# Performance work log

Measured on AMD Instinct MI355X. Metric: run time of the kernel, lower is better.

Reference implementation:

```python
import math
import jax, jax.numpy as jnp
import numpy as np

H = 12
D_MODEL = 768
D_K = D_MODEL // H
B, S = 2, 2048


def setup_inputs() -> dict:
    key = jax.random.key(0)
    ks = jax.random.split(key, 12)
    sc = 0.02
    inp = {
        "query": jax.random.normal(ks[0], (B, S, D_MODEL), jnp.float32),
        "key": jax.random.normal(ks[1], (B, S, D_MODEL), jnp.float32),
        "value": jax.random.normal(ks[2], (B, S, D_MODEL), jnp.float32),
        # causal mask [B, S, S]: 1 where attendable
        "mask": jnp.broadcast_to(jnp.tril(jnp.ones((S, S), jnp.int32)), (B, S, S)),
        "Wq": sc * jax.random.normal(ks[3], (D_MODEL, D_MODEL), jnp.float32),
        "bq": jnp.zeros((D_MODEL,), jnp.float32),
        "Wk": sc * jax.random.normal(ks[4], (D_MODEL, D_MODEL), jnp.float32),
        "bk": jnp.zeros((D_MODEL,), jnp.float32),
        "Wv": sc * jax.random.normal(ks[5], (D_MODEL, D_MODEL), jnp.float32),
        "bv": jnp.zeros((D_MODEL,), jnp.float32),
        "Wo": sc * jax.random.normal(ks[6], (D_MODEL, D_MODEL), jnp.float32),
        "bo": jnp.zeros((D_MODEL,), jnp.float32),
    }
    return inp


def reference(query, key, value, mask, Wq, bq, Wk, bk, Wv, bv, Wo, bo):
    b, s, _ = query.shape
    # linear projections (torch Linear: x @ W.T + b), split into heads
    def proj(x, W, bias):
        return (x @ W.T + bias).reshape(b, s, H, D_K).transpose(0, 2, 1, 3)  # [B,H,S,Dk]

    q = proj(query, Wq, bq)
    k = proj(key, Wk, bk)
    v = proj(value, Wv, bv)

    scores = jnp.einsum("bhqd,bhkd->bhqk", q, k) / math.sqrt(D_K)  # [B,H,S,S]
    # exponential time-decay bias over key positions 1..S, shape [1,1,1,S]
    time = jnp.exp(-jnp.arange(1, s + 1, dtype=scores.dtype))[None, None, None, :]
    scores = jnp.where(mask[:, None, :, :] == 0, jnp.asarray(-1e9, scores.dtype), scores)
    p_attn = jax.nn.softmax(scores - time, axis=-1)
    x = jnp.einsum("bhqk,bhkd->bhqd", p_attn, v)  # [B,H,S,Dk]
    x = x.transpose(0, 2, 1, 3).reshape(b, s, H * D_K)
    return x @ Wo.T + bo
```

## Files before the change

kernel.cpp:

```cpp
#include <hip/hip_runtime.h>
#include <hip/hip_bf16.h>
#include <math.h>

typedef __bf16 bf16;
typedef __attribute__((ext_vector_type(8))) __bf16 bf16x8;
typedef __attribute__((ext_vector_type(4))) float floatx4;

#define NH 12
#define DK 64
#define DM 768
#define NB 2
#define SEQ 2048
#define MTOT (NB * SEQ)
#define WELEM (DM * DM)

static __device__ __forceinline__ bf16x8 load8(const bf16* p) {
    return *(const bf16x8*)p;
}
static __device__ __forceinline__ float4 ld4(const float* p) {
    return *(const float4*)p;
}
static __device__ __forceinline__ bf16x8 cvt8(const float4 a, const float4 b) {
    bf16x8 r;
    r[0] = (bf16)a.x; r[1] = (bf16)a.y; r[2] = (bf16)a.z; r[3] = (bf16)a.w;
    r[4] = (bf16)b.x; r[5] = (bf16)b.y; r[6] = (bf16)b.z; r[7] = (bf16)b.w;
    return r;
}
static __device__ __forceinline__ void async16(const bf16* g, bf16* l) {
    __builtin_amdgcn_global_load_lds((const __attribute__((address_space(1))) void*)g,
                                     (__attribute__((address_space(3))) void*)l,
                                     16, 0, 0);
}

__global__ __launch_bounds__(256) void cvtw_kernel(const float* __restrict__ wq,
                                                   const float* __restrict__ wk,
                                                   const float* __restrict__ wv,
                                                   const float* __restrict__ wo,
                                                   bf16* __restrict__ dst,
                                                   bf16* __restrict__ wob) {
    const int g = blockIdx.x * 256 + threadIdx.x;
    const int PW = WELEM / 8;
    const int wi = g / PW;
    const int rem = g - wi * PW;
    const int n = rem / 96;
    const int t = rem - n * 96;
    const int s = t >> 3;
    const int j = t & 7;
    const float* src = (wi == 0) ? wq : (wi == 1) ? wk : (wi == 2) ? wv : wo;
    bf16* dbase = (wi < 3) ? (dst + (size_t)wi * WELEM) : wob;
    const float* p = src + (size_t)n * DM + s * 64 + j * 8;
    bf16* d = dbase + (size_t)n * DM + s * 64 + ((j ^ (n & 7)) * 8);
    *(bf16x8*)d = cvt8(ld4(p), ld4(p + 4));
}

__global__ __launch_bounds__(256, 3) void qkv_kernel(
    const float* __restrict__ Xq, const float* __restrict__ Xk, const float* __restrict__ Xv,
    const bf16* __restrict__ Wb,
    const float* __restrict__ bq, const float* __restrict__ bk, const float* __restrict__ bv,
    bf16* __restrict__ Oq, bf16* __restrict__ Ok, bf16* __restrict__ Ov) {
    __shared__ bf16 As[128][72];
    __shared__ bf16 Bs[2][128 * 64];

    const int tid = threadIdx.x;
    const int id = blockIdx.x;
    const int xcd = id & 7;
    const int sl = id >> 3;
    const int z = sl / 24;
    const int rr = sl % 24;
    const int m0 = (xcd * 4 + rr / 6) * 128;
    const int n0 = (rr % 6) * 128;

    const float* X = (z == 0) ? Xq : (z == 1) ? Xk : Xv;
    const bf16* W = Wb + (size_t)z * WELEM;
    const float* bias = (z == 0) ? bq : (z == 1) ? bk : bv;
    bf16* out = (z == 0) ? Oq : (z == 1) ? Ok : Ov;
    const int omode = (z == 2) ? 1 : 0;

    const int wv = tid >> 6;
    const int wm = wv >> 1, wn = wv & 1;
    const int lane = tid & 63;
    const int ln = lane & 15;
    const int kq = lane >> 4;
    const int arow = tid >> 1;
    const int acol = (tid & 1) * 32;

    const float* xbase = &X[(size_t)(m0 + arow) * DM + acol];
    const int brow_l = lane >> 3;
    const int bcol_l = (lane & 7) * 8;

    floatx4 acc[4][4];
#pragma unroll
    for (int i = 0; i < 4; i++)
#pragma unroll
        for (int j = 0; j < 4; j++) acc[i][j] = (floatx4){0.f, 0.f, 0.f, 0.f};

    float4 ax[8];
#pragma unroll
    for (int q = 0; q < 8; q++) ax[q] = ld4(xbase + q * 4);
#pragma unroll
    for (int it = 0; it < 4; it++) {
        const bf16* g = W + (size_t)(n0 + it * 32 + wv * 8 + brow_l) * DM + bcol_l;
        async16(g, &Bs[0][(it * 32 + wv * 8) * 64]);
    }

    for (int k = 0; k < 12; k++) {
        const int k0 = k * 64;
        __syncthreads();
        *(bf16x8*)&As[arow][acol]      = cvt8(ax[0], ax[1]);
        *(bf16x8*)&As[arow][acol + 8]  = cvt8(ax[2], ax[3]);
        *(bf16x8*)&As[arow][acol + 16] = cvt8(ax[4], ax[5]);
        *(bf16x8*)&As[arow][acol + 24] = cvt8(ax[6], ax[7]);
        __syncthreads();
        if (k < 11) {
            const float* xp = xbase + k0 + 64;
#pragma unroll
            for (int q = 0; q < 8; q++) ax[q] = ld4(xp + q * 4);
            const int p = (k + 1) & 1;
#pragma unroll
            for (int it = 0; it < 4; it++) {
                const bf16* g = W + (size_t)(n0 + it * 32 + wv * 8 + brow_l) * DM + (k0 + 64) + bcol_l;
                async16(g, &Bs[p][(it * 32 + wv * 8) * 64]);
            }
        }
        const bf16* Bp = &Bs[k & 1][0];
#pragma unroll
        for (int ks = 0; ks < 2; ks++) {
            bf16x8 af[4], bfm[4];
#pragma unroll
            for (int mt = 0; mt < 4; mt++) af[mt] = *(bf16x8*)&As[wm * 64 + mt * 16 + ln][ks * 32 + kq * 8];
#pragma unroll
            for (int nt = 0; nt < 4; nt++) {
                const int brow = wn * 64 + nt * 16 + ln;
                const int jb = (ks * 4 + kq) ^ (ln & 7);
                bfm[nt] = *(const bf16x8*)&Bp[brow * 64 + jb * 8];
            }
#pragma unroll
            for (int mt = 0; mt < 4; mt++)
#pragma unroll
                for (int nt = 0; nt < 4; nt++)
                    acc[mt][nt] = __builtin_amdgcn_mfma_f32_16x16x32_bf16(af[mt], bfm[nt], acc[mt][nt], 0, 0, 0);
        }
    }

    bf16 (*E)[136] = (bf16(*)[136])As;
    float bv4[4];
#pragma unroll
    for (int nt = 0; nt < 4; nt++) bv4[nt] = bias[n0 + wn * 64 + nt * 16 + ln];
    const int erow = tid >> 2;
    const int ecol = (tid & 3) * 32;

    if (omode == 0) {
        const int b = m0 >> 11;
#pragma unroll
        for (int half = 0; half < 2; half++) {
            __syncthreads();
            if (wm == half) {
#pragma unroll
                for (int mt = 0; mt < 4; mt++)
#pragma unroll
                    for (int nt = 0; nt < 4; nt++)
#pragma unroll
                        for (int r2 = 0; r2 < 4; r2++)
                            E[mt * 16 + kq * 4 + r2][wn * 64 + nt * 16 + ln] = (bf16)(acc[mt][nt][r2] + bv4[nt]);
            }
            __syncthreads();
            const int m = m0 + half * 64 + erow;
            const int ss = m & (SEQ - 1);
#pragma unroll
            for (int g = 0; g < 2; g++) {
                const int c = ecol + g * 16;
                const int n = n0 + c;
                const int h = n >> 6, d = n & 63;
                bf16* op = &out[((size_t)(b * NH + h) * SEQ + ss) * DK + d];
                *(bf16x8*)op = *(bf16x8*)&E[erow][c];
                *(bf16x8*)(op + 8) = *(bf16x8*)&E[erow][c + 8];
            }
        }
    } else {
        const int b = m0 >> 11;
        const int s0 = m0 & (SEQ - 1);
#pragma unroll
        for (int half = 0; half < 2; half++) {
            __syncthreads();
            if (wn == half) {
#pragma unroll
                for (int nt = 0; nt < 4; nt++)
#pragma unroll
                    for (int mt = 0; mt < 4; mt++) {
#pragma unroll
                        for (int r2 = 0; r2 < 4; r2++)
                            E[nt * 16 + ln][wm * 64 + mt * 16 + kq * 4 + r2] = (bf16)(acc[mt][nt][r2] + bv4[nt]);
                    }
            }
            __syncthreads();
            const int n = n0 + half * 64 + erow;
            const int h = n >> 6, d = n & 63;
            bf16* op = &out[(size_t)(b * NH + h) * DK * SEQ + (size_t)d * SEQ + s0 + ecol];
            *(bf16x8*)op = *(bf16x8*)&E[erow][ecol];
            *(bf16x8*)(op + 8) = *(bf16x8*)&E[erow][ecol + 8];
            *(bf16x8*)(op + 16) = *(bf16x8*)&E[erow][ecol + 16];
            *(bf16x8*)(op + 24) = *(bf16x8*)&E[erow][ecol + 24];
        }
    }
}

__global__ __launch_bounds__(256) void attn_kernel(const bf16* __restrict__ Q,
                                                   const bf16* __restrict__ K,
                                                   const bf16* __restrict__ Vt,
                                                   bf16* __restrict__ Xout) {
    __shared__ bf16 Ks[128][72];
    __shared__ bf16 Vs[64][136];
    __shared__ bf16 Ps[4][16][136];

    const int tid = threadIdx.x;
    const int wv = tid >> 6;
    const int lane = tid & 63;
    const int ln = lane & 15;
    const int kq = lane >> 4;
    const int krow = tid >> 1;
    const int kcol = (tid & 1) * 32;
    const int vrow = tid >> 2;
    const int vcol = (tid & 3) * 32;

    const int bidx = blockIdx.x;
    const int rk = (bidx < 256 || bidx >= 512) ? bidx : 767 - bidx;
    const int x = 31 - (rk / 24);
    const int bh = rk % 24;

    const int q0 = x * 64;
    const int qbase = q0 + wv * 16;
    const int nch = (x >> 1) + 1;

    const bf16* Qb = Q + (size_t)bh * SEQ * DK;
    const bf16* Kb = K + (size_t)bh * SEQ * DK;
    const bf16* Vb = Vt + (size_t)bh * SEQ * DK;

    const bf16x8 qa0 = load8(&Qb[(size_t)(qbase + ln) * DK + kq * 8]);
    const bf16x8 qa1 = load8(&Qb[(size_t)(qbase + ln) * DK + 32 + kq * 8]);

    bf16x8 kx[4], vx[4];
#pragma unroll
    for (int q = 0; q < 4; q++) {
        kx[q] = load8(&Kb[(size_t)krow * DK + kcol + q * 8]);
        vx[q] = load8(&Vb[(size_t)vrow * SEQ + vcol + q * 8]);
    }

    float lsum[4] = {0.f, 0.f, 0.f, 0.f};
    floatx4 Oacc[4];
#pragma unroll
    for (int nt = 0; nt < 4; nt++) Oacc[nt] = (floatx4){0.f, 0.f, 0.f, 0.f};

    int qg[4];
#pragma unroll
    for (int r = 0; r < 4; r++) qg[r] = qbase + kq * 4 + r;

    for (int c = 0; c < nch; c++) {
        const int k0 = c * 128;
        __syncthreads();
#pragma unroll
        for (int q = 0; q < 4; q++) {
            *(bf16x8*)&Ks[krow][kcol + q * 8] = kx[q];
            *(bf16x8*)&Vs[vrow][vcol + q * 8] = vx[q];
        }
        __syncthreads();
        if (c + 1 < nch) {
            const int kn = k0 + 128;
#pragma unroll
            for (int q = 0; q < 4; q++) {
                kx[q] = load8(&Kb[(size_t)(kn + krow) * DK + kcol + q * 8]);
                vx[q] = load8(&Vb[(size_t)vrow * SEQ + kn + vcol + q * 8]);
            }
        }

        floatx4 sc[8];
#pragma unroll
        for (int ks = 0; ks < 8; ks++) {
            const bf16x8 b0 = *(bf16x8*)&Ks[ks * 16 + ln][kq * 8];
            const bf16x8 b1 = *(bf16x8*)&Ks[ks * 16 + ln][32 + kq * 8];
            floatx4 t = (floatx4){0.f, 0.f, 0.f, 0.f};
            t = __builtin_amdgcn_mfma_f32_16x16x32_bf16(qa0, b0, t, 0, 0, 0);
            t = __builtin_amdgcn_mfma_f32_16x16x32_bf16(qa1, b1, t, 0, 0, 0);
            sc[ks] = t;
        }

        const bool last = (c == nch - 1);
#pragma unroll
        for (int ks = 0; ks < 8; ks++) {
            const int kg = k0 + ks * 16 + ln;
            const float tb = __expf(-(float)(kg + 1));
#pragma unroll
            for (int r = 0; r < 4; r++) {
                const float sv = sc[ks][r] * 0.125f - tb;
                float pf = __expf(sv);
                if (last && kg > qg[r]) pf = 0.f;
                const bf16 pb = (bf16)pf;
                Ps[wv][kq * 4 + r][ks * 16 + ln] = pb;
                lsum[r] += (float)pb;
            }
        }

        bf16x8 pa[4];
#pragma unroll
        for (int seg = 0; seg < 4; seg++) pa[seg] = *(bf16x8*)&Ps[wv][ln][seg * 32 + kq * 8];
#pragma unroll
        for (int nt = 0; nt < 4; nt++) {
#pragma unroll
            for (int seg = 0; seg < 4; seg++) {
                const bf16x8 vb = *(bf16x8*)&Vs[nt * 16 + ln][seg * 32 + kq * 8];
                Oacc[nt] = __builtin_amdgcn_mfma_f32_16x16x32_bf16(pa[seg], vb, Oacc[nt], 0, 0, 0);
            }
        }
    }

#pragma unroll
    for (int off = 1; off < 16; off <<= 1) {
#pragma unroll
        for (int r = 0; r < 4; r++) lsum[r] += __shfl_xor(lsum[r], off, 64);
    }
    float rl[4];
#pragma unroll
    for (int r = 0; r < 4; r++) rl[r] = 1.f / lsum[r];

    __syncthreads();
    bf16 (*E)[72] = (bf16(*)[72])Ks;
    const int erow = tid >> 2;
    const int ecb = (tid & 3) * 16;
#pragma unroll
    for (int nt = 0; nt < 4; nt++) {
#pragma unroll
        for (int r = 0; r < 4; r++)
            E[wv * 16 + kq * 4 + r][nt * 16 + ln] = (bf16)(Oacc[nt][r] * rl[r]);
    }
    __syncthreads();
    const int b = bh / NH;
    const int h = bh - b * NH;
    const int q = q0 + erow;
    bf16* op = &Xout[((size_t)(b * SEQ + q)) * DM + h * DK + ecb];
    *(bf16x8*)op = *(bf16x8*)&E[erow][ecb];
    *(bf16x8*)(op + 8) = *(bf16x8*)&E[erow][ecb + 8];
}

__global__ __launch_bounds__(256, 3) void outproj_kernel(const bf16* __restrict__ X,
                                                         const bf16* __restrict__ W,
                                                         const float* __restrict__ bias,
                                                         float* __restrict__ out) {
    __shared__ bf16 As[128][72];
    __shared__ bf16 Bs[2][128 * 64];

    const int tid = threadIdx.x;
    const int id = blockIdx.x;
    const int xcd = id & 7;
    const int sl = id >> 3;
    const int m0 = (xcd * 4 + sl / 6) * 128;
    const int n0 = (sl % 6) * 128;

    const int wv = tid >> 6;
    const int wm = wv >> 1, wn = wv & 1;
    const int lane = tid & 63;
    const int ln = lane & 15;
    const int kq = lane >> 4;
    const int arow = tid >> 1;
    const int acol = (tid & 1) * 32;

    const bf16* xbase = &X[(size_t)(m0 + arow) * DM + acol];
    const int brow_l = lane >> 3;
    const int bcol_l = (lane & 7) * 8;

    floatx4 acc[4][4];
#pragma unroll
    for (int i = 0; i < 4; i++)
#pragma unroll
        for (int j = 0; j < 4; j++) acc[i][j] = (floatx4){0.f, 0.f, 0.f, 0.f};

    bf16x8 ax[4];
#pragma unroll
    for (int q = 0; q < 4; q++) ax[q] = load8(xbase + q * 8);
#pragma unroll
    for (int it = 0; it < 4; it++) {
        const bf16* g = W + (size_t)(n0 + it * 32 + wv * 8 + brow_l) * DM + bcol_l;
        async16(g, &Bs[0][(it * 32 + wv * 8) * 64]);
    }

    for (int k = 0; k < 12; k++) {
        const int k0 = k * 64;
        __syncthreads();
        *(bf16x8*)&As[arow][acol]      = ax[0];
        *(bf16x8*)&As[arow][acol + 8]  = ax[1];
        *(bf16x8*)&As[arow][acol + 16] = ax[2];
        *(bf16x8*)&As[arow][acol + 24] = ax[3];
        __syncthreads();
        if (k < 11) {
            const bf16* xp = xbase + k0 + 64;
#pragma unroll
            for (int q = 0; q < 4; q++) ax[q] = load8(xp + q * 8);
            const int p = (k + 1) & 1;
#pragma unroll
            for (int it = 0; it < 4; it++) {
                const bf16* g = W + (size_t)(n0 + it * 32 + wv * 8 + brow_l) * DM + (k0 + 64) + bcol_l;
                async16(g, &Bs[p][(it * 32 + wv * 8) * 64]);
            }
        }
        const bf16* Bp = &Bs[k & 1][0];
#pragma unroll
        for (int ks = 0; ks < 2; ks++) {
            bf16x8 af[4], bfm[4];
#pragma unroll
            for (int mt = 0; mt < 4; mt++) af[mt] = *(bf16x8*)&As[wm * 64 + mt * 16 + ln][ks * 32 + kq * 8];
#pragma unroll
            for (int nt = 0; nt < 4; nt++) {
                const int brow = wn * 64 + nt * 16 + ln;
                const int jb = (ks * 4 + kq) ^ (ln & 7);
                bfm[nt] = *(const bf16x8*)&Bp[brow * 64 + jb * 8];
            }
#pragma unroll
            for (int mt = 0; mt < 4; mt++)
#pragma unroll
                for (int nt = 0; nt < 4; nt++)
                    acc[mt][nt] = __builtin_amdgcn_mfma_f32_16x16x32_bf16(af[mt], bfm[nt], acc[mt][nt], 0, 0, 0);
        }
    }

#pragma unroll
    for (int nt = 0; nt < 4; nt++) {
        const int n = n0 + wn * 64 + nt * 16 + ln;
        const float bval = bias[n];
#pragma unroll
        for (int mt = 0; mt < 4; mt++)
#pragma unroll
            for (int r2 = 0; r2 < 4; r2++) {
                const int m = m0 + wm * 64 + mt * 16 + kq * 4 + r2;
                out[(size_t)m * DM + n] = acc[mt][nt][r2] + bval;
            }
    }
}

extern "C" void kernel_launch(void* const* d_in, const int* in_sizes, int n_in,
                              void* d_out, int out_size, void* d_ws, size_t ws_size,
                              hipStream_t stream) {
    const float* query = (const float*)d_in[0];
    const float* key   = (const float*)d_in[1];
    const float* value = (const float*)d_in[2];
    const float* Wq = (const float*)d_in[4];
    const float* bq = (const float*)d_in[5];
    const float* Wk = (const float*)d_in[6];
    const float* bk = (const float*)d_in[7];
    const float* Wv = (const float*)d_in[8];
    const float* bv = (const float*)d_in[9];
    const float* Wo = (const float*)d_in[10];
    const float* bo = (const float*)d_in[11];
    float* out = (float*)d_out;

    const size_t nElem = (size_t)NB * NH * SEQ * DK;
    bf16* Qws  = (bf16*)d_ws;
    bf16* Kws  = Qws + nElem;
    bf16* Vtws = Kws + nElem;
    bf16* Xws  = Vtws + nElem;
    bf16* Wob  = Xws + (size_t)MTOT * DM;

    bf16* Wb = (bf16*)out;

    cvtw_kernel<<<(4 * WELEM / 8) / 256, 256, 0, stream>>>(Wq, Wk, Wv, Wo, Wb, Wob);

    qkv_kernel<<<576, 256, 0, stream>>>(query, key, value, Wb, bq, bk, bv,
                                        Qws, Kws, Vtws);

    attn_kernel<<<768, 256, 0, stream>>>(Qws, Kws, Vtws, Xws);

    outproj_kernel<<<192, 256, 0, stream>>>(Xws, Wob, bo, out);
}
```

Before: 225.3 us.

## Pre-convert activations to bf16 and use async LDS loads with smaller GEMM tiles

Adds the fp32→bf16 conversion of the query/key/value activations to the weight-conversion kernel, writing them with an XOR-swizzled layout. The QKV and output-projection GEMMs can then load both operands straight into LDS with double-buffered global_load_lds, instead of going through registers with a convert step. M tiles shrink from 128 to 64, doubling the grid for better occupancy and balance. The attention epilogue now writes its output swizzled to match the outproj loader. The cost is an extra pass over the activations through workspace, plus smaller tiles that reuse each weight tile less.

```diff
diff --git a/kernel.cpp b/kernel.cpp
--- a/kernel.cpp
+++ b/kernel.cpp
@@ -4,6 +4,7 @@
 
 typedef __bf16 bf16;
 typedef __attribute__((ext_vector_type(8))) __bf16 bf16x8;
+typedef __attribute__((ext_vector_type(4))) __bf16 bf16x4;
 typedef __attribute__((ext_vector_type(4))) float floatx4;
 
 #define NH 12
@@ -13,6 +14,7 @@
 #define SEQ 2048
 #define MTOT (NB * SEQ)
 #define WELEM (DM * DM)
+#define XELEM (MTOT * DM)
 
 static __device__ __forceinline__ bf16x8 load8(const bf16* p) {
     return *(const bf16x8*)p;
@@ -32,175 +34,172 @@
                                      16, 0, 0);
 }
 
-__global__ __launch_bounds__(256) void cvtw_kernel(const float* __restrict__ wq,
-                                                   const float* __restrict__ wk,
-                                                   const float* __restrict__ wv,
-                                                   const float* __restrict__ wo,
-                                                   bf16* __restrict__ dst,
-                                                   bf16* __restrict__ wob) {
+__global__ __launch_bounds__(256) void cvt_kernel(
+    const float* __restrict__ wq, const float* __restrict__ wk,
+    const float* __restrict__ wv, const float* __restrict__ wo,
+    const float* __restrict__ xq, const float* __restrict__ xk, const float* __restrict__ xv,
+    bf16* __restrict__ Wb, bf16* __restrict__ Wob,
+    bf16* __restrict__ Xqb, bf16* __restrict__ Xkb, bf16* __restrict__ Xvb) {
     const int g = blockIdx.x * 256 + threadIdx.x;
     const int PW = WELEM / 8;
-    const int wi = g / PW;
-    const int rem = g - wi * PW;
-    const int n = rem / 96;
-    const int t = rem - n * 96;
-    const int s = t >> 3;
-    const int j = t & 7;
-    const float* src = (wi == 0) ? wq : (wi == 1) ? wk : (wi == 2) ? wv : wo;
-    bf16* dbase = (wi < 3) ? (dst + (size_t)wi * WELEM) : wob;
-    const float* p = src + (size_t)n * DM + s * 64 + j * 8;
-    bf16* d = dbase + (size_t)n * DM + s * 64 + ((j ^ (n & 7)) * 8);
-    *(bf16x8*)d = cvt8(ld4(p), ld4(p + 4));
+    const int PX = XELEM / 8;
+    if (g < 4 * PW) {
+        const int wi = g / PW;
+        const int rem = g - wi * PW;
+        const int n = rem / 96;
+        const int t = rem - n * 96;
+        const int s = t >> 3;
+        const int j = t & 7;
+        const float* src = (wi == 0) ? wq : (wi == 1) ? wk : (wi == 2) ? wv : wo;
+        bf16* dst = (wi < 3) ? (Wb + (size_t)wi * WELEM) : Wob;
+        const float* p = src + (size_t)n * DM + s * 64 + j * 8;
+        *(bf16x8*)(dst + (size_t)n * DM + s * 64 + ((j ^ (n & 7)) * 8)) = cvt8(ld4(p), ld4(p + 4));
+    } else {
+        const int gx = g - 4 * PW;
+        const int xi = gx / PX;
+        const int rem = gx - xi * PX;
+        const int m = rem / 96;
+        const int t = rem - m * 96;
+        const int s = t >> 3;
+        const int j = t & 7;
+        const float* src = (xi == 0) ? xq : (xi == 1) ? xk : xv;
+        bf16* dst = (xi == 0) ? Xqb : (xi == 1) ? Xkb : Xvb;
+        const float* p = src + (size_t)m * DM + s * 64 + j * 8;
+        *(bf16x8*)(dst + (size_t)m * DM + s * 64 + ((j ^ (m & 7)) * 8)) = cvt8(ld4(p), ld4(p + 4));
+    }
 }
 
 __global__ __launch_bounds__(256, 3) void qkv_kernel(
-    const float* __restrict__ Xq, const float* __restrict__ Xk, const float* __restrict__ Xv,
+    const bf16* __restrict__ Xqb, const bf16* __restrict__ Xkb, const bf16* __restrict__ Xvb,
     const bf16* __restrict__ Wb,
     const float* __restrict__ bq, const float* __restrict__ bk, const float* __restrict__ bv,
     bf16* __restrict__ Oq, bf16* __restrict__ Ok, bf16* __restrict__ Ov) {
-    __shared__ bf16 As[128][72];
-    __shared__ bf16 Bs[2][128 * 64];
+    __shared__ __align__(16) bf16 SM[2 * 64 * 64 + 2 * 128 * 64];
+    bf16* As0 = SM;
+    bf16* Bs0 = SM + 8192;
 
     const int tid = threadIdx.x;
     const int id = blockIdx.x;
     const int xcd = id & 7;
     const int sl = id >> 3;
-    const int z = sl / 24;
-    const int rr = sl % 24;
-    const int m0 = (xcd * 4 + rr / 6) * 128;
-    const int n0 = (rr % 6) * 128;
-
-    const float* X = (z == 0) ? Xq : (z == 1) ? Xk : Xv;
+    const int z = sl / 48;
+    const int r = sl % 48;
+    const int m0 = (xcd * 8 + r / 6) * 64;
+    const int n0 = (r % 6) * 128;
+
+    const bf16* X = (z == 0) ? Xqb : (z == 1) ? Xkb : Xvb;
     const bf16* W = Wb + (size_t)z * WELEM;
     const float* bias = (z == 0) ? bq : (z == 1) ? bk : bv;
     bf16* out = (z == 0) ? Oq : (z == 1) ? Ok : Ov;
-    const int omode = (z == 2) ? 1 : 0;
 
     const int wv = tid >> 6;
     const int wm = wv >> 1, wn = wv & 1;
     const int lane = tid & 63;
     const int ln = lane & 15;
     const int kq = lane >> 4;
-    const int arow = tid >> 1;
-    const int acol = (tid & 1) * 32;
-
-    const float* xbase = &X[(size_t)(m0 + arow) * DM + acol];
-    const int brow_l = lane >> 3;
-    const int bcol_l = (lane & 7) * 8;
-
-    floatx4 acc[4][4];
-#pragma unroll
-    for (int i = 0; i < 4; i++)
+    const int drow = lane >> 3;
+    const int dcol = (lane & 7) * 8;
+
+    floatx4 acc[2][4];
+#pragma unroll
+    for (int i = 0; i < 2; i++)
 #pragma unroll
         for (int j = 0; j < 4; j++) acc[i][j] = (floatx4){0.f, 0.f, 0.f, 0.f};
 
-    float4 ax[8];
-#pragma unroll
-    for (int q = 0; q < 8; q++) ax[q] = ld4(xbase + q * 4);
-#pragma unroll
-    for (int it = 0; it < 4; it++) {
-        const bf16* g = W + (size_t)(n0 + it * 32 + wv * 8 + brow_l) * DM + bcol_l;
-        async16(g, &Bs[0][(it * 32 + wv * 8) * 64]);
-    }
+#pragma unroll
+    for (int it = 0; it < 2; it++)
+        async16(X + (size_t)(m0 + wv * 16 + it * 8 + drow) * DM + dcol,
+                As0 + (wv * 16 + it * 8) * 64);
+#pragma unroll
+    for (int it = 0; it < 4; it++)
+        async16(W + (size_t)(n0 + wv * 32 + it * 8 + drow) * DM + dcol,
+                Bs0 + (wv * 32 + it * 8) * 64);
 
     for (int k = 0; k < 12; k++) {
-        const int k0 = k * 64;
-        __syncthreads();
-        *(bf16x8*)&As[arow][acol]      = cvt8(ax[0], ax[1]);
-        *(bf16x8*)&As[arow][acol + 8]  = cvt8(ax[2], ax[3]);
-        *(bf16x8*)&As[arow][acol + 16] = cvt8(ax[4], ax[5]);
-        *(bf16x8*)&As[arow][acol + 24] = cvt8(ax[6], ax[7]);
-        __syncthreads();
+        __syncthreads();
+        const bf16* Ap = As0 + (k & 1) * 4096;
+        const bf16* Bp = Bs0 + (k & 1) * 8192;
         if (k < 11) {
-            const float* xp = xbase + k0 + 64;
-#pragma unroll
-            for (int q = 0; q < 8; q++) ax[q] = ld4(xp + q * 4);
-            const int p = (k + 1) & 1;
-#pragma unroll
-            for (int it = 0; it < 4; it++) {
-                const bf16* g = W + (size_t)(n0 + it * 32 + wv * 8 + brow_l) * DM + (k0 + 64) + bcol_l;
-                async16(g, &Bs[p][(it * 32 + wv * 8) * 64]);
-            }
-        }
-        const bf16* Bp = &Bs[k & 1][0];
+            const int kc = (k + 1) * 64;
+            bf16* An = As0 + ((k + 1) & 1) * 4096;
+            bf16* Bn = Bs0 + ((k + 1) & 1) * 8192;
+#pragma unroll
+            for (int it = 0; it < 2; it++)
+                async16(X + (size_t)(m0 + wv * 16 + it * 8 + drow) * DM + kc + dcol,
+                        An + (wv * 16 + it * 8) * 64);
+#pragma unroll
+            for (int it = 0; it < 4; it++)
+                async16(W + (size_t)(n0 + wv * 32 + it * 8 + drow) * DM + kc + dcol,
+                        Bn + (wv * 32 + it * 8) * 64);
+        }
 #pragma unroll
         for (int ks = 0; ks < 2; ks++) {
-            bf16x8 af[4], bfm[4];
-#pragma unroll
-            for (int mt = 0; mt < 4; mt++) af[mt] = *(bf16x8*)&As[wm * 64 + mt * 16 + ln][ks * 32 + kq * 8];
-#pragma unroll
-            for (int nt = 0; nt < 4; nt++) {
-                const int brow = wn * 64 + nt * 16 + ln;
-                const int jb = (ks * 4 + kq) ^ (ln & 7);
-                bfm[nt] = *(const bf16x8*)&Bp[brow * 64 + jb * 8];
-            }
-#pragma unroll
-            for (int mt = 0; mt < 4; mt++)
+            const int jb = (ks * 4 + kq) ^ (ln & 7);
+            bf16x8 af[2], bfm[4];
+#pragma unroll
+            for (int mt = 0; mt < 2; mt++)
+                af[mt] = *(const bf16x8*)&Ap[(wm * 32 + mt * 16 + ln) * 64 + jb * 8];
+#pragma unroll
+            for (int nt = 0; nt < 4; nt++)
+                bfm[nt] = *(const bf16x8*)&Bp[(wn * 64 + nt * 16 + ln) * 64 + jb * 8];
+#pragma unroll
+            for (int mt = 0; mt < 2; mt++)
 #pragma unroll
                 for (int nt = 0; nt < 4; nt++)
                     acc[mt][nt] = __builtin_amdgcn_mfma_f32_16x16x32_bf16(af[mt], bfm[nt], acc[mt][nt], 0, 0, 0);
         }
     }
 
-    bf16 (*E)[136] = (bf16(*)[136])As;
     float bv4[4];
 #pragma unroll
     for (int nt = 0; nt < 4; nt++) bv4[nt] = bias[n0 + wn * 64 + nt * 16 + ln];
-    const int erow = tid >> 2;
-    const int ecol = (tid & 3) * 32;
-
-    if (omode == 0) {
-        const int b = m0 >> 11;
-#pragma unroll
-        for (int half = 0; half < 2; half++) {
-            __syncthreads();
-            if (wm == half) {
-#pragma unroll
-                for (int mt = 0; mt < 4; mt++)
-#pragma unroll
-                    for (int nt = 0; nt < 4; nt++)
-#pragma unroll
-                        for (int r2 = 0; r2 < 4; r2++)
-                            E[mt * 16 + kq * 4 + r2][wn * 64 + nt * 16 + ln] = (bf16)(acc[mt][nt][r2] + bv4[nt]);
+
+    if (z < 2) {
+        __syncthreads();
+        bf16 (*E)[136] = (bf16(*)[136])SM;
+#pragma unroll
+        for (int mt = 0; mt < 2; mt++)
+#pragma unroll
+            for (int nt = 0; nt < 4; nt++)
+#pragma unroll
+                for (int r2 = 0; r2 < 4; r2++)
+                    E[wm * 32 + mt * 16 + kq * 4 + r2][wn * 64 + nt * 16 + ln] =
+                        (bf16)(acc[mt][nt][r2] + bv4[nt]);
+        __syncthreads();
+        const int row = tid >> 2;
+        const int cb = (tid & 3) * 32;
+        const int m = m0 + row;
+        const int b = m >> 11;
+        const int s = m & (SEQ - 1);
+        const int h = (n0 + cb) >> 6;
+        const int d = (n0 + cb) & 63;
+        bf16* op = &out[((size_t)(b * NH + h) * SEQ + s) * DK + d];
+#pragma unroll
+        for (int q2 = 0; q2 < 4; q2++)
+            *(bf16x8*)(op + q2 * 8) = *(bf16x8*)&E[row][cb + q2 * 8];
+    } else {
+        __syncthreads();
+        bf16 (*E)[72] = (bf16(*)[72])SM;
+#pragma unroll
+        for (int nt = 0; nt < 4; nt++)
+#pragma unroll
+            for (int mt = 0; mt < 2; mt++) {
+                bf16x4 v;
+#pragma unroll
+                for (int r2 = 0; r2 < 4; r2++) v[r2] = (bf16)(acc[mt][nt][r2] + bv4[nt]);
+                *(bf16x4*)&E[wn * 64 + nt * 16 + ln][wm * 32 + mt * 16 + kq * 4] = v;
             }
-            __syncthreads();
-            const int m = m0 + half * 64 + erow;
-            const int ss = m & (SEQ - 1);
-#pragma unroll
-            for (int g = 0; g < 2; g++) {
-                const int c = ecol + g * 16;
-                const int n = n0 + c;
-                const int h = n >> 6, d = n & 63;
-                bf16* op = &out[((size_t)(b * NH + h) * SEQ + ss) * DK + d];
-                *(bf16x8*)op = *(bf16x8*)&E[erow][c];
-                *(bf16x8*)(op + 8) = *(bf16x8*)&E[erow][c + 8];
-            }
-        }
-    } else {
+        __syncthreads();
+        const int row = tid >> 1;
+        const int sc = (tid & 1) * 32;
         const int b = m0 >> 11;
         const int s0 = m0 & (SEQ - 1);
-#pragma unroll
-        for (int half = 0; half < 2; half++) {
-            __syncthreads();
-            if (wn == half) {
-#pragma unroll
-                for (int nt = 0; nt < 4; nt++)
-#pragma unroll
-                    for (int mt = 0; mt < 4; mt++) {
-#pragma unroll
-                        for (int r2 = 0; r2 < 4; r2++)
-                            E[nt * 16 + ln][wm * 64 + mt * 16 + kq * 4 + r2] = (bf16)(acc[mt][nt][r2] + bv4[nt]);
-                    }
-            }
-            __syncthreads();
-            const int n = n0 + half * 64 + erow;
-            const int h = n >> 6, d = n & 63;
-            bf16* op = &out[(size_t)(b * NH + h) * DK * SEQ + (size_t)d * SEQ + s0 + ecol];
-            *(bf16x8*)op = *(bf16x8*)&E[erow][ecol];
-            *(bf16x8*)(op + 8) = *(bf16x8*)&E[erow][ecol + 8];
-            *(bf16x8*)(op + 16) = *(bf16x8*)&E[erow][ecol + 16];
-            *(bf16x8*)(op + 24) = *(bf16x8*)&E[erow][ecol + 24];
-        }
+        const int h = (n0 >> 6) + (row >> 6);
+        const int d = row & 63;
+        bf16* op = &out[(size_t)(b * NH + h) * DK * SEQ + (size_t)d * SEQ + s0 + sc];
+#pragma unroll
+        for (int q2 = 0; q2 < 4; q2++)
+            *(bf16x8*)(op + q2 * 8) = *(bf16x8*)&E[row][sc + q2 * 8];
     }
 }
 
@@ -335,23 +334,26 @@
     const int b = bh / NH;
     const int h = bh - b * NH;
     const int q = q0 + erow;
-    bf16* op = &Xout[((size_t)(b * SEQ + q)) * DM + h * DK + ecb];
-    *(bf16x8*)op = *(bf16x8*)&E[erow][ecb];
-    *(bf16x8*)(op + 8) = *(bf16x8*)&E[erow][ecb + 8];
+    const int j0 = (tid & 3) * 2;
+    const int key = erow & 7;
+    bf16* rowp = &Xout[((size_t)(b * SEQ + q)) * DM + h * DK];
+    *(bf16x8*)(rowp + ((j0 ^ key) * 8)) = *(bf16x8*)&E[erow][ecb];
+    *(bf16x8*)(rowp + (((j0 + 1) ^ key) * 8)) = *(bf16x8*)&E[erow][ecb + 8];
 }
 
 __global__ __launch_bounds__(256, 3) void outproj_kernel(const bf16* __restrict__ X,
                                                          const bf16* __restrict__ W,
                                                          const float* __restrict__ bias,
                                                          float* __restrict__ out) {
-    __shared__ bf16 As[128][72];
-    __shared__ bf16 Bs[2][128 * 64];
+    __shared__ __align__(16) bf16 SM[2 * 64 * 64 + 2 * 128 * 64];
+    bf16* As0 = SM;
+    bf16* Bs0 = SM + 8192;
 
     const int tid = threadIdx.x;
     const int id = blockIdx.x;
     const int xcd = id & 7;
     const int sl = id >> 3;
-    const int m0 = (xcd * 4 + sl / 6) * 128;
+    const int m0 = (xcd * 8 + sl / 6) * 64;
     const int n0 = (sl % 6) * 128;
 
     const int wv = tid >> 6;
@@ -359,61 +361,53 @@
     const int lane = tid & 63;
     const int ln = lane & 15;
     const int kq = lane >> 4;
-    const int arow = tid >> 1;
-    const int acol = (tid & 1) * 32;
-
-    const bf16* xbase = &X[(size_t)(m0 + arow) * DM + acol];
-    const int brow_l = lane >> 3;
-    const int bcol_l = (lane & 7) * 8;
-
-    floatx4 acc[4][4];
-#pragma unroll
-    for (int i = 0; i < 4; i++)
+    const int drow = lane >> 3;
+    const int dcol = (lane & 7) * 8;
+
+    floatx4 acc[2][4];
+#pragma unroll
+    for (int i = 0; i < 2; i++)
 #pragma unroll
         for (int j = 0; j < 4; j++) acc[i][j] = (floatx4){0.f, 0.f, 0.f, 0.f};
 
-    bf16x8 ax[4];
-#pragma unroll
-    for (int q = 0; q < 4; q++) ax[q] = load8(xbase + q * 8);
-#pragma unroll
-    for (int it = 0; it < 4; it++) {
-        const bf16* g = W + (size_t)(n0 + it * 32 + wv * 8 + brow_l) * DM + bcol_l;
-        async16(g, &Bs[0][(it * 32 + wv * 8) * 64]);
-    }
+#pragma unroll
+    for (int it = 0; it < 2; it++)
+        async16(X + (size_t)(m0 + wv * 16 + it * 8 + drow) * DM + dcol,
+                As0 + (wv * 16 + it * 8) * 64);
+#pragma unroll
+    for (int it = 0; it < 4; it++)
+        async16(W + (size_t)(n0 + wv * 32 + it * 8 + drow) * DM + dcol,
+                Bs0 + (wv * 32 + it * 8) * 64);
 
     for (int k = 0; k < 12; k++) {
-        const int k0 = k * 64;
-        __syncthreads();
-        *(bf16x8*)&As[arow][acol]      = ax[0];
-        *(bf16x8*)&As[arow][acol + 8]  = ax[1];
-        *(bf16x8*)&As[arow][acol + 16] = ax[2];
-        *(bf16x8*)&As[arow][acol + 24] = ax[3];
-        __syncthreads();
+        __syncthreads();
+        const bf16* Ap = As0 + (k & 1) * 4096;
+        const bf16* Bp = Bs0 + (k & 1) * 8192;
         if (k < 11) {
-            const bf16* xp = xbase + k0 + 64;
-#pragma unroll
-            for (int q = 0; q < 4; q++) ax[q] = load8(xp + q * 8);
-            const int p = (k + 1) & 1;
-#pragma unroll
-            for (int it = 0; it < 4; it++) {
-                const bf16* g = W + (size_t)(n0 + it * 32 + wv * 8 + brow_l) * DM + (k0 + 64) + bcol_l;
-                async16(g, &Bs[p][(it * 32 + wv * 8) * 64]);
-            }
-        }
-        const bf16* Bp = &Bs[k & 1][0];
+            const int kc = (k + 1) * 64;
+            bf16* An = As0 + ((k + 1) & 1) * 4096;
+            bf16* Bn = Bs0 + ((k + 1) & 1) * 8192;
+#pragma unroll
+            for (int it = 0; it < 2; it++)
+                async16(X + (size_t)(m0 + wv * 16 + it * 8 + drow) * DM + kc + dcol,
+                        An + (wv * 16 + it * 8) * 64);
+#pragma unroll
+            for (int it = 0; it < 4; it++)
+                async16(W + (size_t)(n0 + wv * 32 + it * 8 + drow) * DM + kc + dcol,
+                        Bn + (wv * 32 + it * 8) * 64);
+        }
 #pragma unroll
         for (int ks = 0; ks < 2; ks++) {
-            bf16x8 af[4], bfm[4];
-#pragma unroll
-            for (int mt = 0; mt < 4; mt++) af[mt] = *(bf16x8*)&As[wm * 64 + mt * 16 + ln][ks * 32 + kq * 8];
-#pragma unroll
-            for (int nt = 0; nt < 4; nt++) {
-                const int brow = wn * 64 + nt * 16 + ln;
-                const int jb = (ks * 4 + kq) ^ (ln & 7);
-                bfm[nt] = *(const bf16x8*)&Bp[brow * 64 + jb * 8];
-            }
-#pragma unroll
-            for (int mt = 0; mt < 4; mt++)
+            const int jb = (ks * 4 + kq) ^ (ln & 7);
+            bf16x8 af[2], bfm[4];
+#pragma unroll
+            for (int mt = 0; mt < 2; mt++)
+                af[mt] = *(const bf16x8*)&Ap[(wm * 32 + mt * 16 + ln) * 64 + jb * 8];
+#pragma unroll
+            for (int nt = 0; nt < 4; nt++)
+                bfm[nt] = *(const bf16x8*)&Bp[(wn * 64 + nt * 16 + ln) * 64 + jb * 8];
+#pragma unroll
+            for (int mt = 0; mt < 2; mt++)
 #pragma unroll
                 for (int nt = 0; nt < 4; nt++)
                     acc[mt][nt] = __builtin_amdgcn_mfma_f32_16x16x32_bf16(af[mt], bfm[nt], acc[mt][nt], 0, 0, 0);
@@ -425,10 +419,10 @@
         const int n = n0 + wn * 64 + nt * 16 + ln;
         const float bval = bias[n];
 #pragma unroll
-        for (int mt = 0; mt < 4; mt++)
+        for (int mt = 0; mt < 2; mt++)
 #pragma unroll
             for (int r2 = 0; r2 < 4; r2++) {
-                const int m = m0 + wm * 64 + mt * 16 + kq * 4 + r2;
+                const int m = m0 + wm * 32 + mt * 16 + kq * 4 + r2;
                 out[(size_t)m * DM + n] = acc[mt][nt][r2] + bval;
             }
     }
@@ -450,21 +444,26 @@
     const float* bo = (const float*)d_in[11];
     float* out = (float*)d_out;
 
-    const size_t nElem = (size_t)NB * NH * SEQ * DK;
     bf16* Qws  = (bf16*)d_ws;
-    bf16* Kws  = Qws + nElem;
-    bf16* Vtws = Kws + nElem;
-    bf16* Xws  = Vtws + nElem;
-    bf16* Wob  = Xws + (size_t)MTOT * DM;
-
-    bf16* Wb = (bf16*)out;
-
-    cvtw_kernel<<<(4 * WELEM / 8) / 256, 256, 0, stream>>>(Wq, Wk, Wv, Wo, Wb, Wob);
-
-    qkv_kernel<<<576, 256, 0, stream>>>(query, key, value, Wb, bq, bk, bv,
-                                        Qws, Kws, Vtws);
+    bf16* Kws  = Qws + XELEM;
+    bf16* Vtws = Kws + XELEM;
+    bf16* Xws  = Vtws + XELEM;
+    bf16* Wob  = Xws + XELEM;
+    bf16* Xvb  = Wob + WELEM;
+
+    bf16* Wb  = (bf16*)out;
+    bf16* Xkb = (bf16*)out + 3 * WELEM;
+
+    bf16* Xqb = Xws;
+
+    const int ncvt = (4 * (WELEM / 8) + 3 * (XELEM / 8)) / 256;
+    cvt_kernel<<<ncvt, 256, 0, stream>>>(Wq, Wk, Wv, Wo, query, key, value,
+                                         Wb, Wob, Xqb, Xkb, Xvb);
+
+    qkv_kernel<<<1152, 256, 0, stream>>>(Xqb, Xkb, Xvb, Wb, bq, bk, bv,
+                                         Qws, Kws, Vtws);
 
     attn_kernel<<<768, 256, 0, stream>>>(Qws, Kws, Vtws, Xws);
 
-    outproj_kernel<<<192, 256, 0, stream>>>(Xws, Wob, bo, out);
-}
+    outproj_kernel<<<384, 256, 0, stream>>>(Xws, Wob, bo, out);
+}
```

New measurement: 195.0 us (median of 2 runs). 1.16x faster.
